# Kernel optimization log

Measured on AMD Instinct MI355X. Metric: run time of the kernel, lower is better.

## Reference

```python
import jax, jax.numpy as jnp
import numpy as np

jax.config.update("jax_enable_x64", True)

# config
B, S = 4, 4096
H_SIZE = 2048          # hidden_size
VOCAB = 128000         # engram_base_vocab_size
MAX_NGRAM = 3          # engram_max_ngram_size -> orders 2..3
PRIME = 500009         # engram_n_embed_per_ngram (same prime for every order)
N_HEAD = 4             # engram_n_head_per_ngram
E = 32                 # engram_embed_dim
KS = 4                 # short conv kernel size
NUM_ORDERS = MAX_NGRAM - 1
TOTAL_HEADS = NUM_ORDERS * N_HEAD
TOTAL_ROWS = PRIME * N_HEAD * NUM_ORDERS  # flat multi-head table rows


def setup_inputs() -> dict:
    key = jax.random.key(0)
    k_ids, k_h, k_tab, k_cw, k_hp, k_gp, k_op = jax.random.split(key, 7)
    input_ids = jax.random.randint(k_ids, (B, S), 0, VOCAB, dtype=jnp.int64)
    hidden_states = jax.random.normal(k_h, (B, S, H_SIZE), dtype=jnp.float32)
    # identity compressed-tokenizer mapping buffer
    mapping = jnp.arange(VOCAB, dtype=jnp.int64)
    # deterministic odd multipliers, seeded like _build_multipliers
    rng = np.random.default_rng(0 * 10007 + 0 * 1009)
    mults = rng.integers(1, 2 ** 31, size=(NUM_ORDERS, N_HEAD, MAX_NGRAM))
    multipliers = jnp.asarray(mults * 2 + 1, dtype=jnp.int64)
    table = 0.02 * jax.random.normal(k_tab, (TOTAL_ROWS, E), dtype=jnp.float32)
    conv_w = 0.1 * jax.random.normal(k_cw, (E, KS), dtype=jnp.float32)  # depthwise taps
    conv_b = jnp.zeros((E,), dtype=jnp.float32)
    Wh = 0.05 * jax.random.normal(k_hp, (E, TOTAL_HEADS * E), dtype=jnp.float32)
    Wg = 0.02 * jax.random.normal(k_gp, (E, H_SIZE), dtype=jnp.float32)
    Wo = 0.02 * jax.random.normal(k_op, (H_SIZE, E), dtype=jnp.float32)
    return {"input_ids": input_ids, "hidden_states": hidden_states,
            "mapping": mapping, "multipliers": multipliers, "table": table,
            "conv_w": conv_w, "conv_b": conv_b, "Wh": Wh, "Wg": Wg, "Wo": Wo}


def _hash_indices(compressed, multipliers):
    """XOR-mix n-gram hash indices -> [B, S, TOTAL_HEADS] int64."""
    all_idx = []
    offset = 0
    for oi, k in enumerate(range(2, MAX_NGRAM + 1)):
        # forward sliding window, clamped at last token (matches cat/expand trick)
        pos = jnp.minimum(jnp.arange(S)[:, None] + jnp.arange(k)[None, :], S - 1)  # [S,k]
        ng = compressed[:, pos]                                  # [B,S,k]
        m = multipliers[oi, :, :k]                               # [nh,k]
        prod = ng[:, :, None, :] * m[None, None, :, :]           # [B,S,nh,k]
        h = prod[..., 0]
        for p in range(1, k):
            h = h ^ prod[..., p]
        idx = h % PRIME + (offset + jnp.arange(N_HEAD, dtype=jnp.int64) * PRIME)
        all_idx.append(idx)
        offset += PRIME * N_HEAD
    return jnp.concatenate(all_idx, axis=-1)


def reference(input_ids, hidden_states, mapping, multipliers, table,
              conv_w, conv_b, Wh, Wg, Wo):
    compressed = mapping[input_ids]                              # [B,S]
    indices = _hash_indices(compressed, multipliers)             # [B,S,TOTAL_HEADS]
    emb = table[indices].reshape(B, S, TOTAL_HEADS * E)          # multi-head gather
    emb = emb @ Wh.T                                             # head_proj -> [B,S,E]
    # causal depthwise short conv (kernel KS, left pad KS-1)
    xp = jnp.pad(emb, ((0, 0), (KS - 1, 0), (0, 0)))
    emb = sum(xp[:, j:j + S, :] * conv_w[:, j] for j in range(KS)) + conv_b
    gate = jax.nn.sigmoid(hidden_states @ Wg.T)                  # [B,S,E]
    return (gate * emb) @ Wo.T                                   # [B,S,H_SIZE]
```

## Files before the change

kernel.cpp:

```cpp
#include <hip/hip_runtime.h>
#include <hip/hip_bf16.h>
#include <stdint.h>

#define HSZ 2048
#define PRIME 500009u

typedef __attribute__((ext_vector_type(8))) short short8;
typedef __attribute__((ext_vector_type(4))) float f32x4;
typedef __attribute__((ext_vector_type(4))) unsigned uint4v;
typedef __attribute__((ext_vector_type(2))) unsigned uint2v;

__device__ __forceinline__ unsigned pk2(float x, float y) {
  __hip_bfloat162 h = __float22bfloat162_rn(make_float2(x, y));
  return *reinterpret_cast<unsigned*>(&h);
}
__device__ __forceinline__ short f2bf(float f) {
  __hip_bfloat16 h = __float2bfloat16(f);
  return *reinterpret_cast<short*>(&h);
}
__device__ __forceinline__ short8 pack8(float4 a, float4 b) {
  uint4v u = {pk2(a.x, a.y), pk2(a.z, a.w), pk2(b.x, b.y), pk2(b.z, b.w)};
  return __builtin_bit_cast(short8, u);
}
__device__ __forceinline__ short8 load8_bf(const float* __restrict__ p) {
  float4 a = *reinterpret_cast<const float4*>(p);
  float4 b = *reinterpret_cast<const float4*>(p + 4);
  return pack8(a, b);
}
__device__ __forceinline__ void gload_lds16(const float* g, void* l) {
  __builtin_amdgcn_global_load_lds(
      (const __attribute__((address_space(1))) void*)g,
      (__attribute__((address_space(3))) void*)l, 16, 0, 0);
}

__global__ __launch_bounds__(256) void emb0_kernel(
    const int* __restrict__ ids, const int* __restrict__ mapping,
    const unsigned* __restrict__ mult, const float* __restrict__ table,
    const float* __restrict__ Wh, float* __restrict__ emb0) {
  __shared__ __align__(16) short A_lds[32][264];
  __shared__ int idx_lds[256];
  const int tid = threadIdx.x;
  const int t0 = blockIdx.x * 32;

  {
    int t_loc = tid >> 3, head = tid & 7;
    int tg = t0 + t_loc;
    int b = tg >> 12, s = tg & 4095;
    const int* idb = ids + (b << 12);
    int s1 = s + 1 > 4095 ? 4095 : s + 1;
    int s2 = s + 2 > 4095 ? 4095 : s + 2;
    uint64_t c0 = (unsigned)mapping[idb[s]];
    uint64_t c1 = (unsigned)mapping[idb[s1]];
    uint64_t c2 = (unsigned)mapping[idb[s2]];
    int mb = head * 3;
    uint64_t h = (c0 * (uint64_t)mult[mb]) ^ (c1 * (uint64_t)mult[mb + 1]);
    if (head >= 4) h ^= c2 * (uint64_t)mult[mb + 2];
    unsigned row = (unsigned)(h % PRIME) + (unsigned)head * PRIME;
    idx_lds[tid] = (int)row;
  }
  __syncthreads();

  #pragma unroll
  for (int p = 0; p < 8; ++p) {
    int r = p * 32 + (tid >> 3);
    int c4 = (tid & 7) * 4;
    long row = idx_lds[r];
    float4 v = *reinterpret_cast<const float4*>(table + row * 32 + c4);
    int tl = r >> 3, hd = r & 7;
    uint2v pk = {pk2(v.x, v.y), pk2(v.z, v.w)};
    *reinterpret_cast<uint2v*>(&A_lds[tl][hd * 32 + c4]) = pk;
  }
  __syncthreads();

  int wid = tid >> 6, lane = tid & 63;
  int tt = wid >> 1, e0 = (wid & 1) * 16;
  int l16 = lane & 15, q = lane >> 4;
  short8 Wf[8];
  #pragma unroll
  for (int ks = 0; ks < 8; ++ks)
    Wf[ks] = load8_bf(Wh + (size_t)(e0 + l16) * 256 + ks * 32 + q * 8);
  f32x4 acc = {0.f, 0.f, 0.f, 0.f};
  #pragma unroll
  for (int ks = 0; ks < 8; ++ks) {
    short8 a = *reinterpret_cast<const short8*>(&A_lds[tt * 16 + l16][ks * 32 + q * 8]);
    acc = __builtin_amdgcn_mfma_f32_16x16x32_bf16(Wf[ks], a, acc, 0, 0, 0);
  }
  int t = t0 + tt * 16 + l16;
  *reinterpret_cast<f32x4*>(&emb0[(size_t)t * 32 + e0 + q * 4]) = acc;
}

__global__ __launch_bounds__(256) void fuse_kernel(
    const float* __restrict__ hidden, const float* __restrict__ emb0,
    const float* __restrict__ cw, const float* __restrict__ cb,
    const float* __restrict__ Wg, const float* __restrict__ Wo,
    float* __restrict__ out) {
  __shared__ __align__(16) float hbuf[2][32][256];
  __shared__ float emb_lds[32][33];
  __shared__ __align__(16) short ge_lds[32][40];
  const int tid = threadIdx.x;
  const int wid = tid >> 6, lane = tid & 63;
  const int l16 = lane & 15, q = lane >> 4;
  const int t0 = blockIdx.x * 32;

  auto STAGE = [&](int buf, int kc) {
    #pragma unroll
    for (int j = 0; j < 8; ++j) {
      int r = wid * 8 + j;
      unsigned so = ((unsigned)(lane * 16) ^ (((unsigned)r & 7) << 4)) >> 2;
      const float* src = hidden + (size_t)(t0 + r) * HSZ + kc * 256 + so;
      gload_lds16(src, &hbuf[buf][r][0]);
    }
  };

  STAGE(0, 0);

  #pragma unroll
  for (int it = 0; it < 4; ++it) {
    int ii = it * 256 + tid;
    int tl = ii >> 5, e = ii & 31;
    int s = (t0 + tl) & 4095;
    float a = cb[e];
    #pragma unroll
    for (int j = 0; j < 4; ++j) {
      int sp = s - 3 + j;
      if (sp >= 0) a += cw[e * 4 + j] * emb0[(size_t)(t0 + tl - 3 + j) * 32 + e];
    }
    emb_lds[tl][e] = a;
  }
  __syncthreads();

  const int tt = wid >> 1, ee = wid & 1;
  const int R = tt * 16 + l16;
  const unsigned sw = ((unsigned)R & 7) << 4;
  const char* hrow0 = (const char*)&hbuf[0][0][0] + R * 1024;
  const char* hrow1 = (const char*)&hbuf[1][0][0] + R * 1024;
  const float* wgp = Wg + (size_t)(ee * 16 + l16) * HSZ + q * 8;
  f32x4 acc = {0.f, 0.f, 0.f, 0.f};
  for (int kc = 0; kc < 8; ++kc) {
    if (kc < 7) STAGE((kc + 1) & 1, kc + 1);
    const char* hb = (kc & 1) ? hrow1 : hrow0;
    short8 A[8], B[8];
    #pragma unroll
    for (int ks = 0; ks < 8; ++ks) {
      B[ks] = load8_bf(wgp + kc * 256 + ks * 32);
      unsigned b0 = (unsigned)(ks * 128 + q * 32);
      float4 a0 = *reinterpret_cast<const float4*>(hb + (b0 ^ sw));
      float4 a1 = *reinterpret_cast<const float4*>(hb + ((b0 + 16) ^ sw));
      A[ks] = pack8(a0, a1);
    }
    #pragma unroll
    for (int ks = 0; ks < 8; ++ks)
      acc = __builtin_amdgcn_mfma_f32_16x16x32_bf16(A[ks], B[ks], acc, 0, 0, 0);
    __syncthreads();
  }

  #pragma unroll
  for (int j = 0; j < 4; ++j) {
    int r = tt * 16 + q * 4 + j, c = ee * 16 + l16;
    float g = 1.f / (1.f + __expf(-acc[j]));
    ge_lds[r][c] = f2bf(g * emb_lds[r][c]);
  }
  __syncthreads();

  short8 Af0 = *reinterpret_cast<const short8*>(&ge_lds[l16][q * 8]);
  short8 Af1 = *reinterpret_cast<const short8*>(&ge_lds[16 + l16][q * 8]);
  float* orow0 = out + (size_t)(t0 + l16) * HSZ;
  float* orow1 = out + (size_t)(t0 + 16 + l16) * HSZ;
  int hbase = wid * 512;
  for (int ht = 0; ht < 32; ++ht) {
    int h0 = hbase + ht * 16;
    short8 aw = load8_bf(Wo + (size_t)(h0 + l16) * 32 + q * 8);
    f32x4 z = {0, 0, 0, 0};
    f32x4 o0 = __builtin_amdgcn_mfma_f32_16x16x32_bf16(aw, Af0, z, 0, 0, 0);
    f32x4 o1 = __builtin_amdgcn_mfma_f32_16x16x32_bf16(aw, Af1, z, 0, 0, 0);
    *reinterpret_cast<f32x4*>(orow0 + h0 + q * 4) = o0;
    *reinterpret_cast<f32x4*>(orow1 + h0 + q * 4) = o1;
  }
}

extern "C" void kernel_launch(void* const* d_in, const int* in_sizes, int n_in,
                              void* d_out, int out_size, void* d_ws, size_t ws_size,
                              hipStream_t stream) {
  const int* ids = (const int*)d_in[0];
  const float* hidden = (const float*)d_in[1];
  const int* mapping = (const int*)d_in[2];
  const unsigned* mult = (const unsigned*)d_in[3];
  const float* table = (const float*)d_in[4];
  const float* cw = (const float*)d_in[5];
  const float* cb = (const float*)d_in[6];
  const float* Wh = (const float*)d_in[7];
  const float* Wg = (const float*)d_in[8];
  const float* Wo = (const float*)d_in[9];
  float* out = (float*)d_out;
  float* emb0 = (float*)d_ws;

  emb0_kernel<<<512, 256, 0, stream>>>(ids, mapping, mult, table, Wh, emb0);
  fuse_kernel<<<512, 256, 0, stream>>>(hidden, emb0, cw, cb, Wg, Wo, out);
}
```

Measured before the change: 90.78 us.

## Fuse embedding gather/projection into main kernel with halo recompute and finer pipeline

Merges the two kernels into one. Each block recomputes hashes, gathers and head-projects 48 tokens, a 16-token halo plus its own 32, so the causal conv no longer needs a global emb0 buffer or a second launch. The hidden-state staging changes from 8 chunks of 256 columns to 32 chunks of 64 columns, with two chunks issued ahead and explicit vmcnt/lgkm waits plus raw s_barrier calls. This cuts LDS use to allow 2 blocks per CU, at the cost of redundant halo work and far more barriers per block.

```diff
diff --git a/kernel.cpp b/kernel.cpp
--- a/kernel.cpp
+++ b/kernel.cpp
@@ -4,12 +4,19 @@
 
 #define HSZ 2048
 #define PRIME 500009u
+#define CHUNK 64
+#define NCH 32
 
 typedef __attribute__((ext_vector_type(8))) short short8;
 typedef __attribute__((ext_vector_type(4))) float f32x4;
 typedef __attribute__((ext_vector_type(4))) unsigned uint4v;
 typedef __attribute__((ext_vector_type(2))) unsigned uint2v;
 
+#define MEMFENCE asm volatile("" ::: "memory")
+#define BARRIER() do { MEMFENCE; __builtin_amdgcn_s_barrier(); MEMFENCE; } while (0)
+#define WAIT_LGKM0 asm volatile("s_waitcnt lgkmcnt(0)" ::: "memory")
+#define WAIT_VM(n) asm volatile("s_waitcnt vmcnt(" #n ")" ::: "memory")
+
 __device__ __forceinline__ unsigned pk2(float x, float y) {
   __hip_bfloat162 h = __float22bfloat162_rn(make_float2(x, y));
   return *reinterpret_cast<unsigned*>(&h);
@@ -33,134 +40,145 @@
       (__attribute__((address_space(3))) void*)l, 16, 0, 0);
 }
 
-__global__ __launch_bounds__(256) void emb0_kernel(
+__global__ __launch_bounds__(256, 2) void engram_fused(
     const int* __restrict__ ids, const int* __restrict__ mapping,
     const unsigned* __restrict__ mult, const float* __restrict__ table,
-    const float* __restrict__ Wh, float* __restrict__ emb0) {
-  __shared__ __align__(16) short A_lds[32][264];
-  __shared__ int idx_lds[256];
-  const int tid = threadIdx.x;
-  const int t0 = blockIdx.x * 32;
-
-  {
-    int t_loc = tid >> 3, head = tid & 7;
-    int tg = t0 + t_loc;
-    int b = tg >> 12, s = tg & 4095;
-    const int* idb = ids + (b << 12);
-    int s1 = s + 1 > 4095 ? 4095 : s + 1;
-    int s2 = s + 2 > 4095 ? 4095 : s + 2;
-    uint64_t c0 = (unsigned)mapping[idb[s]];
-    uint64_t c1 = (unsigned)mapping[idb[s1]];
-    uint64_t c2 = (unsigned)mapping[idb[s2]];
-    int mb = head * 3;
-    uint64_t h = (c0 * (uint64_t)mult[mb]) ^ (c1 * (uint64_t)mult[mb + 1]);
-    if (head >= 4) h ^= c2 * (uint64_t)mult[mb + 2];
-    unsigned row = (unsigned)(h % PRIME) + (unsigned)head * PRIME;
-    idx_lds[tid] = (int)row;
-  }
-  __syncthreads();
-
-  #pragma unroll
-  for (int p = 0; p < 8; ++p) {
-    int r = p * 32 + (tid >> 3);
-    int c4 = (tid & 7) * 4;
-    long row = idx_lds[r];
-    float4 v = *reinterpret_cast<const float4*>(table + row * 32 + c4);
-    int tl = r >> 3, hd = r & 7;
-    uint2v pk = {pk2(v.x, v.y), pk2(v.z, v.w)};
-    *reinterpret_cast<uint2v*>(&A_lds[tl][hd * 32 + c4]) = pk;
-  }
-  __syncthreads();
-
-  int wid = tid >> 6, lane = tid & 63;
-  int tt = wid >> 1, e0 = (wid & 1) * 16;
-  int l16 = lane & 15, q = lane >> 4;
-  short8 Wf[8];
-  #pragma unroll
-  for (int ks = 0; ks < 8; ++ks)
-    Wf[ks] = load8_bf(Wh + (size_t)(e0 + l16) * 256 + ks * 32 + q * 8);
-  f32x4 acc = {0.f, 0.f, 0.f, 0.f};
-  #pragma unroll
-  for (int ks = 0; ks < 8; ++ks) {
-    short8 a = *reinterpret_cast<const short8*>(&A_lds[tt * 16 + l16][ks * 32 + q * 8]);
-    acc = __builtin_amdgcn_mfma_f32_16x16x32_bf16(Wf[ks], a, acc, 0, 0, 0);
-  }
-  int t = t0 + tt * 16 + l16;
-  *reinterpret_cast<f32x4*>(&emb0[(size_t)t * 32 + e0 + q * 4]) = acc;
-}
-
-__global__ __launch_bounds__(256) void fuse_kernel(
-    const float* __restrict__ hidden, const float* __restrict__ emb0,
+    const float* __restrict__ Wh, const float* __restrict__ hidden,
     const float* __restrict__ cw, const float* __restrict__ cb,
     const float* __restrict__ Wg, const float* __restrict__ Wo,
     float* __restrict__ out) {
-  __shared__ __align__(16) float hbuf[2][32][256];
-  __shared__ float emb_lds[32][33];
+  __shared__ __align__(16) float hbuf[2][32][CHUNK];
+  __shared__ __align__(16) short A_lds[48][264];
+  __shared__ __align__(16) float emb48[48][36];
+  __shared__ float emb_c[32][33];
   __shared__ __align__(16) short ge_lds[32][40];
+  __shared__ int idx_lds[384];
+
   const int tid = threadIdx.x;
   const int wid = tid >> 6, lane = tid & 63;
   const int l16 = lane & 15, q = lane >> 4;
   const int t0 = blockIdx.x * 32;
 
   auto STAGE = [&](int buf, int kc) {
-    #pragma unroll
-    for (int j = 0; j < 8; ++j) {
-      int r = wid * 8 + j;
-      unsigned so = ((unsigned)(lane * 16) ^ (((unsigned)r & 7) << 4)) >> 2;
-      const float* src = hidden + (size_t)(t0 + r) * HSZ + kc * 256 + so;
-      gload_lds16(src, &hbuf[buf][r][0]);
+#pragma unroll
+    for (int j = 0; j < 2; ++j) {
+      int r = wid * 8 + j * 4 + (lane >> 4);
+      unsigned c4 = (((unsigned)l16 * 16u) ^ (((unsigned)r & 7u) << 4)) >> 2;
+      const float* src = hidden + (size_t)(t0 + r) * HSZ + kc * CHUNK + c4;
+      gload_lds16(src, &hbuf[buf][wid * 8 + j * 4][0]);
     }
   };
 
   STAGE(0, 0);
-
-  #pragma unroll
+  STAGE(1, 1);
+
+#pragma unroll
+  for (int p = 0; p < 2; ++p) {
+    int hh = p * 256 + tid;
+    if (hh < 384) {
+      int slot = hh >> 3, head = hh & 7;
+      int tg = t0 - 16 + slot;
+      if (tg < 0) tg = 0;
+      int b = tg >> 12, s = tg & 4095;
+      const int* idb = ids + (b << 12);
+      int s1 = s + 1 > 4095 ? 4095 : s + 1;
+      int s2 = s + 2 > 4095 ? 4095 : s + 2;
+      uint64_t c0 = (unsigned)mapping[idb[s]];
+      uint64_t c1 = (unsigned)mapping[idb[s1]];
+      uint64_t c2 = (unsigned)mapping[idb[s2]];
+      int mb = head * 3;
+      uint64_t h = (c0 * (uint64_t)mult[mb]) ^ (c1 * (uint64_t)mult[mb + 1]);
+      if (head >= 4) h ^= c2 * (uint64_t)mult[mb + 2];
+      idx_lds[hh] = (int)((unsigned)(h % PRIME) + (unsigned)head * PRIME);
+    }
+  }
+  WAIT_LGKM0; BARRIER();
+
+#pragma unroll
+  for (int p = 0; p < 12; ++p) {
+    int r = p * 32 + (tid >> 3);
+    int c4 = (tid & 7) * 4;
+    int row = idx_lds[r];
+    float4 v = *reinterpret_cast<const float4*>(table + (size_t)row * 32 + c4);
+    uint2v pk = {pk2(v.x, v.y), pk2(v.z, v.w)};
+    *reinterpret_cast<uint2v*>(&A_lds[r >> 3][(r & 7) * 32 + c4]) = pk;
+  }
+  WAIT_LGKM0; BARRIER();
+
+  for (int job = wid; job < 6; job += 4) {
+    int jt = job >> 1, e0 = (job & 1) * 16;
+    f32x4 acc = {0.f, 0.f, 0.f, 0.f};
+#pragma unroll
+    for (int ks = 0; ks < 8; ++ks) {
+      short8 wf = load8_bf(Wh + (size_t)(e0 + l16) * 256 + ks * 32 + q * 8);
+      short8 a = *reinterpret_cast<const short8*>(&A_lds[jt * 16 + l16][ks * 32 + q * 8]);
+      acc = __builtin_amdgcn_mfma_f32_16x16x32_bf16(wf, a, acc, 0, 0, 0);
+    }
+    *reinterpret_cast<f32x4*>(&emb48[jt * 16 + l16][e0 + q * 4]) = acc;
+  }
+  WAIT_LGKM0; BARRIER();
+
+#pragma unroll
   for (int it = 0; it < 4; ++it) {
     int ii = it * 256 + tid;
     int tl = ii >> 5, e = ii & 31;
-    int s = (t0 + tl) & 4095;
+    int s = (t0 & 4095) + tl;
     float a = cb[e];
-    #pragma unroll
-    for (int j = 0; j < 4; ++j) {
-      int sp = s - 3 + j;
-      if (sp >= 0) a += cw[e * 4 + j] * emb0[(size_t)(t0 + tl - 3 + j) * 32 + e];
-    }
-    emb_lds[tl][e] = a;
-  }
-  __syncthreads();
+#pragma unroll
+    for (int j = 0; j < 4; ++j)
+      if (s - 3 + j >= 0) a += cw[e * 4 + j] * emb48[13 + tl + j][e];
+    emb_c[tl][e] = a;
+  }
+  WAIT_LGKM0; BARRIER();
 
   const int tt = wid >> 1, ee = wid & 1;
   const int R = tt * 16 + l16;
-  const unsigned sw = ((unsigned)R & 7) << 4;
-  const char* hrow0 = (const char*)&hbuf[0][0][0] + R * 1024;
-  const char* hrow1 = (const char*)&hbuf[1][0][0] + R * 1024;
+  const unsigned sw = ((unsigned)R & 7u) << 4;
+  const char* hb0 = (const char*)&hbuf[0][R][0];
+  const char* hb1 = (const char*)&hbuf[1][R][0];
   const float* wgp = Wg + (size_t)(ee * 16 + l16) * HSZ + q * 8;
   f32x4 acc = {0.f, 0.f, 0.f, 0.f};
-  for (int kc = 0; kc < 8; ++kc) {
-    if (kc < 7) STAGE((kc + 1) & 1, kc + 1);
-    const char* hb = (kc & 1) ? hrow1 : hrow0;
-    short8 A[8], B[8];
-    #pragma unroll
-    for (int ks = 0; ks < 8; ++ks) {
-      B[ks] = load8_bf(wgp + kc * 256 + ks * 32);
-      unsigned b0 = (unsigned)(ks * 128 + q * 32);
-      float4 a0 = *reinterpret_cast<const float4*>(hb + (b0 ^ sw));
-      float4 a1 = *reinterpret_cast<const float4*>(hb + ((b0 + 16) ^ sw));
-      A[ks] = pack8(a0, a1);
-    }
-    #pragma unroll
-    for (int ks = 0; ks < 8; ++ks)
-      acc = __builtin_amdgcn_mfma_f32_16x16x32_bf16(A[ks], B[ks], acc, 0, 0, 0);
-    __syncthreads();
-  }
-
-  #pragma unroll
+
+  for (int kc = 0; kc < NCH - 1; ++kc) {
+    WAIT_VM(8);
+    BARRIER();
+    const char* hb = (kc & 1) ? hb1 : hb0;
+    unsigned x0 = q * 32u;
+    float4 a0 = *reinterpret_cast<const float4*>(hb + (x0 ^ sw));
+    float4 a1 = *reinterpret_cast<const float4*>(hb + ((x0 + 16) ^ sw));
+    float4 a2 = *reinterpret_cast<const float4*>(hb + ((x0 + 128) ^ sw));
+    float4 a3 = *reinterpret_cast<const float4*>(hb + ((x0 + 144) ^ sw));
+    short8 A0 = pack8(a0, a1);
+    short8 A1 = pack8(a2, a3);
+    short8 B0 = load8_bf(wgp + kc * CHUNK);
+    short8 B1 = load8_bf(wgp + kc * CHUNK + 32);
+    WAIT_LGKM0;
+    BARRIER();
+    if (kc < NCH - 2) STAGE(kc & 1, kc + 2);
+    acc = __builtin_amdgcn_mfma_f32_16x16x32_bf16(A0, B0, acc, 0, 0, 0);
+    acc = __builtin_amdgcn_mfma_f32_16x16x32_bf16(A1, B1, acc, 0, 0, 0);
+  }
+  {
+    WAIT_VM(0);
+    BARRIER();
+    unsigned x0 = q * 32u;
+    float4 a0 = *reinterpret_cast<const float4*>(hb1 + (x0 ^ sw));
+    float4 a1 = *reinterpret_cast<const float4*>(hb1 + ((x0 + 16) ^ sw));
+    float4 a2 = *reinterpret_cast<const float4*>(hb1 + ((x0 + 128) ^ sw));
+    float4 a3 = *reinterpret_cast<const float4*>(hb1 + ((x0 + 144) ^ sw));
+    short8 B0 = load8_bf(wgp + (NCH - 1) * CHUNK);
+    short8 B1 = load8_bf(wgp + (NCH - 1) * CHUNK + 32);
+    acc = __builtin_amdgcn_mfma_f32_16x16x32_bf16(pack8(a0, a1), B0, acc, 0, 0, 0);
+    acc = __builtin_amdgcn_mfma_f32_16x16x32_bf16(pack8(a2, a3), B1, acc, 0, 0, 0);
+  }
+
+#pragma unroll
   for (int j = 0; j < 4; ++j) {
     int r = tt * 16 + q * 4 + j, c = ee * 16 + l16;
     float g = 1.f / (1.f + __expf(-acc[j]));
-    ge_lds[r][c] = f2bf(g * emb_lds[r][c]);
-  }
-  __syncthreads();
+    ge_lds[r][c] = f2bf(g * emb_c[r][c]);
+  }
+  WAIT_LGKM0; BARRIER();
 
   short8 Af0 = *reinterpret_cast<const short8*>(&ge_lds[l16][q * 8]);
   short8 Af1 = *reinterpret_cast<const short8*>(&ge_lds[16 + l16][q * 8]);
@@ -170,7 +188,7 @@
   for (int ht = 0; ht < 32; ++ht) {
     int h0 = hbase + ht * 16;
     short8 aw = load8_bf(Wo + (size_t)(h0 + l16) * 32 + q * 8);
-    f32x4 z = {0, 0, 0, 0};
+    f32x4 z = {0.f, 0.f, 0.f, 0.f};
     f32x4 o0 = __builtin_amdgcn_mfma_f32_16x16x32_bf16(aw, Af0, z, 0, 0, 0);
     f32x4 o1 = __builtin_amdgcn_mfma_f32_16x16x32_bf16(aw, Af1, z, 0, 0, 0);
     *reinterpret_cast<f32x4*>(orow0 + h0 + q * 4) = o0;
@@ -192,8 +210,7 @@
   const float* Wg = (const float*)d_in[8];
   const float* Wo = (const float*)d_in[9];
   float* out = (float*)d_out;
-  float* emb0 = (float*)d_ws;
-
-  emb0_kernel<<<512, 256, 0, stream>>>(ids, mapping, mult, table, Wh, emb0);
-  fuse_kernel<<<512, 256, 0, stream>>>(hidden, emb0, cw, cb, Wg, Wo, out);
-}
+
+  engram_fused<<<512, 256, 0, stream>>>(ids, mapping, mult, table, Wh, hidden,
+                                        cw, cb, Wg, Wo, out);
+}
```

Result: faster. 79.03 us (-12.9%).
